# Kernel tuning notes

Hardware: AMD Instinct MI355X
Metric: run time of the kernel (lower is better)

## Reference

```python
import jax, jax.numpy as jnp
import numpy as np

# Config matching init_kwargs: lat_size=512, fin=64, fout=64, fhidden=128,
# dim=2, kernel_size=1, stride=1, padding=0, groups=1, lat_factor=1.
B, FIN, FOUT, FHID, H, W = 16, 64, 64, 128, 128, 128
LAT = 512
LS = 512            # self.lat_size (lat_size > 3 so unchanged) * lat_factor
HID1 = 1024         # LinearResidualBlock default hidden = fin + fout
HID2 = 1024         # second LRB hidden = self.lat_size * lat_factor * 2
SIZES = [FHID*FIN, FHID*FHID, FOUT*FHID, FOUT*FIN, FHID, FHID, FOUT, FOUT]
KTOT = int(np.sum(SIZES))  # 37248
OFFS = np.cumsum([0] + SIZES)


def setup_inputs() -> dict:
    key = jax.random.key(0)
    ks = jax.random.split(key, 10)
    def w(k, shape):
        return (jax.random.normal(k, shape, jnp.float32) / np.sqrt(shape[0])).astype(jnp.float32)
    return {
        "x": jax.random.normal(ks[0], (B, FIN, H, W), jnp.float32),
        "lat": jax.random.normal(ks[1], (B, LAT), jnpp := jnp.float32) if False else jax.random.normal(ks[1], (B, LAT), jnp.float32),
        # dyna_k = Linear(LAT, LS) -> LRB(LS, LS) -> LRB(LS, KTOT, hidden=HID2)
        "dk_w": w(ks[2], (LAT, LS)), "dk_b": jnp.zeros((LS,), jnp.float32),
        "l1_w1": w(ks[3], (LS, HID1)), "l1_b1": jnp.zeros((HID1,), jnp.float32),
        "l1_w2": w(ks[4], (HID1, LS)), "l1_b2": jnp.zeros((LS,), jnp.float32),
        "l2_w1": w(ks[5], (LS, HID2)), "l2_b1": jnp.zeros((HID2,), jnp.float32),
        "l2_w2": w(ks[6], (HID2, KTOT)), "l2_b2": jnp.zeros((KTOT,), jnp.float32),
        "l2_ws": w(ks[7], (LS, KTOT)),  # shortcut linear (fin != fout)
    }


def _lrb(h, w1, b1, w2, b2, ws=None):
    # LinearResidualBlock: shortcut(h) + Linear(ReLU(Linear(h)))
    sc = h if ws is None else h @ ws
    return sc + jax.nn.relu(h @ w1 + b1) @ w2 + b2


def _hyper(lat, dk_w, dk_b, l1_w1, l1_b1, l1_w2, l1_b2, l2_w1, l2_b1, l2_w2, l2_b2, l2_ws):
    h = lat @ dk_w + dk_b
    h = _lrb(h, l1_w1, l1_b1, l1_w2, l1_b2)          # fin == fout -> identity shortcut
    return _lrb(h, l2_w1, l2_b1, l2_w2, l2_b2, l2_ws)


def _dyna_block(x, ksv):
    # Split hypernet output into per-sample 1x1 conv kernels and biases.
    k_in = ksv[:, OFFS[0]:OFFS[1]].reshape(B, FHID, FIN)
    k_mid = ksv[:, OFFS[1]:OFFS[2]].reshape(B, FHID, FHID)
    k_out = ksv[:, OFFS[2]:OFFS[3]].reshape(B, FOUT, FHID)
    k_sh = ksv[:, OFFS[3]:OFFS[4]].reshape(B, FOUT, FIN)
    b_in = ksv[:, OFFS[4]:OFFS[5]][:, :, None, None]
    b_mid = ksv[:, OFFS[5]:OFFS[6]][:, :, None, None]
    b_out = ksv[:, OFFS[6]:OFFS[7]][:, :, None, None]
    b_sh = ksv[:, OFFS[7]:OFFS[8]][:, :, None, None]
    # groups = batch trick == per-sample 1x1 conv == batched channel GEMM
    xs = jnp.einsum('boi,bihw->bohw', k_sh, x) + b_sh
    hh = jax.nn.relu(jnp.einsum('boi,bihw->bohw', k_in, x) + b_in)
    hh = jax.nn.relu(jnp.einsum('boi,bihw->bohw', k_mid, hh) + b_mid)
    return jnp.einsum('boi,bihw->bohw', k_out, hh) + b_out + xs


def reference(x, lat, dk_w, dk_b, l1_w1, l1_b1, l1_w2, l1_b2, l2_w1, l2_b1, l2_w2, l2_b2, l2_ws):
    ksv = _hyper(lat, dk_w, dk_b, l1_w1, l1_b1, l1_w2, l1_b2, l2_w1, l2_b1, l2_w2, l2_b2, l2_ws)
    return _dyna_block(x, ksv)  # [B, FOUT, H, W]
```

## Files before the change

kernel.cpp:

```cpp
#include <hip/hip_runtime.h>

#define N_KSV 37248
#define N_KW  36864

typedef float f32x4 __attribute__((ext_vector_type(4)));
typedef short short8 __attribute__((ext_vector_type(8)));
typedef short short4v __attribute__((ext_vector_type(4)));
typedef __bf16 bf16x8 __attribute__((ext_vector_type(8)));

__device__ inline short f2bs(float f) {
  unsigned u = __builtin_bit_cast(unsigned, f);
  u += 0x7fffu + ((u >> 16) & 1u);
  return (short)(u >> 16);
}

__device__ inline f32x4 ntl4(const float* p) {
  return __builtin_nontemporal_load(reinterpret_cast<const f32x4*>(p));
}

__device__ inline f32x4 mfma16(short8 a, short8 b, f32x4 c) {
  return __builtin_amdgcn_mfma_f32_16x16x32_bf16(
      __builtin_bit_cast(bf16x8, a), __builtin_bit_cast(bf16x8, b), c, 0, 0, 0);
}

__global__ void k_h0(const float* __restrict__ lat, const float* __restrict__ w,
                     const float* __restrict__ bias, float* __restrict__ h0) {
  int j = blockIdx.x * 256 + threadIdx.x;
  int b = blockIdx.y;
  const float* lp = lat + b * 512;
  float acc = bias[j];
#pragma unroll 16
  for (int k = 0; k < 512; ++k) acc = fmaf(lp[k], w[k * 512 + j], acc);
  h0[b * 512 + j] = acc;
}

__global__ void k_t1(const float* __restrict__ h0, const float* __restrict__ w,
                     const float* __restrict__ bias, float* __restrict__ t1) {
  int j = blockIdx.x * 256 + threadIdx.x;
  int b = blockIdx.y;
  const float* hp = h0 + b * 512;
  float acc = bias[j];
#pragma unroll 16
  for (int k = 0; k < 512; ++k) acc = fmaf(hp[k], w[k * 1024 + j], acc);
  t1[b * 1024 + j] = fmaxf(acc, 0.f);
}

__global__ void k_h(const float* __restrict__ h0, const float* __restrict__ t1,
                    const float* __restrict__ w, const float* __restrict__ bias,
                    float* __restrict__ h, short* __restrict__ hxT) {
  int j = blockIdx.x * 256 + threadIdx.x;
  int b = blockIdx.y;
  const float* tp = t1 + b * 1024;
  float acc = bias[j];
#pragma unroll 16
  for (int k = 0; k < 1024; ++k) acc = fmaf(tp[k], w[k * 512 + j], acc);
  float v = acc + h0[b * 512 + j];
  h[b * 512 + j] = v;
  hxT[b * 1536 + j] = f2bs(v);
}

__global__ void k_t2(const float* __restrict__ h, const float* __restrict__ w,
                     const float* __restrict__ bias, short* __restrict__ hxT) {
  int j = blockIdx.x * 256 + threadIdx.x;
  int b = blockIdx.y;
  const float* hp = h + b * 512;
  float acc = bias[j];
#pragma unroll 16
  for (int k = 0; k < 512; ++k) acc = fmaf(hp[k], w[k * 1024 + j], acc);
  hxT[b * 1536 + 512 + j] = f2bs(fmaxf(acc, 0.f));
}

#define LOADB(dst, ktv) { \
    const float* bp_ = ((ktv) < 16) ? (wsp + (size_t)((ktv) * 32) * N_KSV) \
                                    : (w2p + (size_t)((ktv) * 32 - 512) * N_KSV); \
    dst[0] = *reinterpret_cast<const f32x4*>(bp_); \
    dst[1] = *reinterpret_cast<const f32x4*>(bp_ + (size_t)1 * N_KSV); \
    dst[2] = *reinterpret_cast<const f32x4*>(bp_ + (size_t)2 * N_KSV); \
    dst[3] = *reinterpret_cast<const f32x4*>(bp_ + (size_t)3 * N_KSV); \
    dst[4] = *reinterpret_cast<const f32x4*>(bp_ + (size_t)4 * N_KSV); \
    dst[5] = *reinterpret_cast<const f32x4*>(bp_ + (size_t)5 * N_KSV); \
    dst[6] = *reinterpret_cast<const f32x4*>(bp_ + (size_t)6 * N_KSV); \
    dst[7] = *reinterpret_cast<const f32x4*>(bp_ + (size_t)7 * N_KSV); }

#define LOADA(dst, ktv) \
    dst = *reinterpret_cast<const short8*>(apb + (ktv) * 32);

#define COMPUTE(bsrc, asrc) { \
    _Pragma("unroll") \
    for (int t = 0; t < 4; ++t) { \
      short8 bf_; \
      bf_[0] = f2bs(bsrc[0][t]); bf_[1] = f2bs(bsrc[1][t]); \
      bf_[2] = f2bs(bsrc[2][t]); bf_[3] = f2bs(bsrc[3][t]); \
      bf_[4] = f2bs(bsrc[4][t]); bf_[5] = f2bs(bsrc[5][t]); \
      bf_[6] = f2bs(bsrc[6][t]); bf_[7] = f2bs(bsrc[7][t]); \
      acc[t] = mfma16(asrc, bf_, acc[t]); \
    } }

__global__ __launch_bounds__(256, 4) void k5_mfma(
    const float* __restrict__ wsm, const float* __restrict__ w2,
    const short* __restrict__ hxT, const float* __restrict__ b2,
    float* __restrict__ ksv, short* __restrict__ kwb) {
  __shared__ f32x4 red[3][64][4];
  const int tid = threadIdx.x;
  const int wv = tid >> 6;
  const int lane = tid & 63;
  const int col0 = blockIdx.x * 64;
  const int l15 = lane & 15;
  const int lg = lane >> 4;

  const float* wsp = wsm + (size_t)(lg * 8) * N_KSV + col0 + l15 * 4;
  const float* w2p = w2 + (size_t)(lg * 8) * N_KSV + col0 + l15 * 4;
  const short* apb = hxT + l15 * 1536 + lg * 8;

  f32x4 acc[4];
#pragma unroll
  for (int t = 0; t < 4; ++t) acc[t] = (f32x4){0.f, 0.f, 0.f, 0.f};

  const int kt0 = wv * 12;
  f32x4 bA[8], bB[8];
  short8 aA, aB;
  LOADB(bA, kt0);
  LOADA(aA, kt0);

#pragma unroll
  for (int s = 0; s < 12; ++s) {
    if (s + 1 < 12) {
      if ((s & 1) == 0) {
        LOADB(bB, kt0 + s + 1);
        LOADA(aB, kt0 + s + 1);
      } else {
        LOADB(bA, kt0 + s + 1);
        LOADA(aA, kt0 + s + 1);
      }
    }
    if ((s & 1) == 0) COMPUTE(bA, aA) else COMPUTE(bB, aB)
  }

  if (wv > 0) {
#pragma unroll
    for (int t = 0; t < 4; ++t) red[wv - 1][lane][t] = acc[t];
  }
  __syncthreads();
  if (wv != 0) return;

#pragma unroll
  for (int t = 0; t < 4; ++t) {
    acc[t] += red[0][lane][t];
    acc[t] += red[1][lane][t];
    acc[t] += red[2][lane][t];
  }

  const int m0 = lg * 4;
#pragma unroll
  for (int t = 0; t < 4; ++t) {
    const int col = col0 + l15 * 4 + t;
    const float bias = b2[col];
#pragma unroll
    for (int r = 0; r < 4; ++r) {
      float s = acc[t][r] + bias;
      ksv[(size_t)(m0 + r) * N_KSV + col] = s;
      if (col < N_KW)
        kwb[(size_t)(m0 + r) * N_KW + col] = f2bs(s);
    }
  }
}

__device__ inline int xT_idx(int p, int c) {
  return p * 64 + ((((c >> 3) ^ (p & 7)) << 3) | (c & 7));
}
__device__ inline int h_idx(int p, int c) {
  return p * 128 + ((((c >> 3) ^ (p & 7)) << 3) | (c & 7));
}

__device__ __forceinline__ void dyna_L1(const short* xT, short* h1s,
    const short* kw, const float* bias, int w, int l15, int lg) {
  short8 a1[2][2];
#pragma unroll
  for (int mt = 0; mt < 2; ++mt)
#pragma unroll
    for (int kf = 0; kf < 2; ++kf)
      a1[mt][kf] = *reinterpret_cast<const short8*>(
          kw + (w * 32 + mt * 16 + l15) * 64 + kf * 32 + lg * 8);

  f32x4 acc1[2][4];
#pragma unroll
  for (int mt = 0; mt < 2; ++mt)
#pragma unroll
    for (int nt = 0; nt < 4; ++nt) acc1[mt][nt] = (f32x4){0.f, 0.f, 0.f, 0.f};

#pragma unroll
  for (int nt = 0; nt < 4; ++nt) {
    int p = nt * 16 + l15;
    short8 b0 = *reinterpret_cast<const short8*>(&xT[xT_idx(p, lg * 8)]);
    short8 b1 = *reinterpret_cast<const short8*>(&xT[xT_idx(p, 32 + lg * 8)]);
#pragma unroll
    for (int mt = 0; mt < 2; ++mt) {
      acc1[mt][nt] = mfma16(a1[mt][0], b0, acc1[mt][nt]);
      acc1[mt][nt] = mfma16(a1[mt][1], b1, acc1[mt][nt]);
    }
  }
#pragma unroll
  for (int mt = 0; mt < 2; ++mt) {
    int ch0 = w * 32 + mt * 16 + lg * 4;
    f32x4 bv = *reinterpret_cast<const f32x4*>(bias + ch0);
#pragma unroll
    for (int nt = 0; nt < 4; ++nt) {
      int p = nt * 16 + l15;
      short4v hv;
#pragma unroll
      for (int jj = 0; jj < 4; ++jj)
        hv[jj] = f2bs(fmaxf(acc1[mt][nt][jj] + bv[jj], 0.f));
      *reinterpret_cast<short4v*>(&h1s[h_idx(p, ch0)]) = hv;
    }
  }
}

__device__ __forceinline__ void dyna_L2(const short* h1s, short* h2s,
    const short* kw, const float* bias, int w, int l15, int lg) {
  short8 a2[2][4];
#pragma unroll
  for (int mt = 0; mt < 2; ++mt)
#pragma unroll
    for (int kf = 0; kf < 4; ++kf)
      a2[mt][kf] = *reinterpret_cast<const short8*>(
          kw + 8192 + (w * 32 + mt * 16 + l15) * 128 + kf * 32 + lg * 8);

  f32x4 acc2[2][4];
#pragma unroll
  for (int mt = 0; mt < 2; ++mt)
#pragma unroll
    for (int nt = 0; nt < 4; ++nt) acc2[mt][nt] = (f32x4){0.f, 0.f, 0.f, 0.f};

#pragma unroll
  for (int nt = 0; nt < 4; ++nt) {
    int p = nt * 16 + l15;
    short8 bb[4];
#pragma unroll
    for (int kf = 0; kf < 4; ++kf)
      bb[kf] = *reinterpret_cast<const short8*>(&h1s[h_idx(p, kf * 32 + lg * 8)]);
#pragma unroll
    for (int mt = 0; mt < 2; ++mt)
#pragma unroll
      for (int kf = 0; kf < 4; ++kf)
        acc2[mt][nt] = mfma16(a2[mt][kf], bb[kf], acc2[mt][nt]);
  }
#pragma unroll
  for (int mt = 0; mt < 2; ++mt) {
    int ch0 = w * 32 + mt * 16 + lg * 4;
    f32x4 bv = *reinterpret_cast<const f32x4*>(bias + 128 + ch0);
#pragma unroll
    for (int nt = 0; nt < 4; ++nt) {
      int p = nt * 16 + l15;
      short4v hv;
#pragma unroll
      for (int jj = 0; jj < 4; ++jj)
        hv[jj] = f2bs(fmaxf(acc2[mt][nt][jj] + bv[jj], 0.f));
      *reinterpret_cast<short4v*>(&h2s[h_idx(p, ch0)]) = hv;
    }
  }
}

__device__ __forceinline__ void dyna_L3(const short* h2s, const short* xT,
    const short* kw, const float* bias, float* outb, int pos0,
    int w, int l15, int lg) {
  short8 a3[4], ash[2];
#pragma unroll
  for (int kf = 0; kf < 4; ++kf)
    a3[kf] = *reinterpret_cast<const short8*>(
        kw + 24576 + (w * 16 + l15) * 128 + kf * 32 + lg * 8);
#pragma unroll
  for (int kf = 0; kf < 2; ++kf)
    ash[kf] = *reinterpret_cast<const short8*>(
        kw + 32768 + (w * 16 + l15) * 64 + kf * 32 + lg * 8);

  int ch0 = w * 16 + lg * 4;
  f32x4 bo = *reinterpret_cast<const f32x4*>(bias + 256 + ch0);
  f32x4 bs = *reinterpret_cast<const f32x4*>(bias + 320 + ch0);

#pragma unroll
  for (int nt = 0; nt < 4; ++nt) {
    int p = nt * 16 + l15;
    f32x4 acc = {0.f, 0.f, 0.f, 0.f};
#pragma unroll
    for (int kf = 0; kf < 4; ++kf) {
      short8 bb = *reinterpret_cast<const short8*>(&h2s[h_idx(p, kf * 32 + lg * 8)]);
      acc = mfma16(a3[kf], bb, acc);
    }
#pragma unroll
    for (int kf = 0; kf < 2; ++kf) {
      short8 bb = *reinterpret_cast<const short8*>(&xT[xT_idx(p, kf * 32 + lg * 8)]);
      acc = mfma16(ash[kf], bb, acc);
    }
#pragma unroll
    for (int jj = 0; jj < 4; ++jj)
      __builtin_nontemporal_store(acc[jj] + bo[jj] + bs[jj],
          outb + (((size_t)(ch0 + jj)) << 14) + pos0 + p);
  }
}

__global__ __launch_bounds__(256) void k_dyna(const float* __restrict__ x,
                                              const short* __restrict__ kwb,
                                              const float* __restrict__ ksv,
                                              float* __restrict__ out) {
  __shared__ __align__(16) short lds[24576];
  short* xTA = lds;
  short* xTB = lds + 4096;
  short* h1s = lds + 8192;
  short* h2s = lds + 16384;

  const int tid = threadIdx.x;
  const int lane = tid & 63;
  const int w = tid >> 6;
  const int l15 = lane & 15;
  const int lg = lane >> 4;

  const int b = blockIdx.x >> 7;
  const int pos0A = (blockIdx.x & 127) << 7;
  const int pos0B = pos0A + 64;

  const float* xb = x + ((size_t)b << 20);
  const short* kw = kwb + b * N_KW;
  const float* bias = ksv + (size_t)b * N_KSV + N_KW;
  float* outb = out + ((size_t)b << 20);

  const int cc = (tid >> 3) * 2;
  const int p0 = (tid & 7) * 8;
  const float* xrow = xb + (size_t)cc * 16384 + p0;

  f32x4 a0 = ntl4(xrow + pos0A),        a1v = ntl4(xrow + pos0A + 4);
  f32x4 a2v = ntl4(xrow + 16384 + pos0A), a3v = ntl4(xrow + 16384 + pos0A + 4);
  f32x4 b0 = ntl4(xrow + pos0B),        b1v = ntl4(xrow + pos0B + 4);
  f32x4 b2v = ntl4(xrow + 16384 + pos0B), b3v = ntl4(xrow + 16384 + pos0B + 4);

#define WRITEX(xT, r0, r1, r2, r3) { \
    _Pragma("unroll") \
    for (int i = 0; i < 8; ++i) { \
      float va = (i < 4) ? r0[i] : r1[i - 4]; \
      float vb = (i < 4) ? r2[i] : r3[i - 4]; \
      int pk = (int)(unsigned short)f2bs(va) | ((int)f2bs(vb) << 16); \
      *reinterpret_cast<int*>(&(xT)[xT_idx(p0 + i, cc)]) = pk; \
    } }

  WRITEX(xTA, a0, a1v, a2v, a3v);
  __syncthreads();

  dyna_L1(xTA, h1s, kw, bias, w, l15, lg);
  __syncthreads();
  dyna_L2(h1s, h2s, kw, bias, w, l15, lg);
  WRITEX(xTB, b0, b1v, b2v, b3v);
  __syncthreads();
  dyna_L3(h2s, xTA, kw, bias, outb, pos0A, w, l15, lg);
  dyna_L1(xTB, h1s, kw, bias, w, l15, lg);
  __syncthreads();
  dyna_L2(h1s, h2s, kw, bias, w, l15, lg);
  __syncthreads();
  dyna_L3(h2s, xTB, kw, bias, outb, pos0B, w, l15, lg);
#undef WRITEX
}

extern "C" void kernel_launch(void* const* d_in, const int* in_sizes, int n_in,
                              void* d_out, int out_size, void* d_ws, size_t ws_size,
                              hipStream_t stream) {
  const float* x    = (const float*)d_in[0];
  const float* lat  = (const float*)d_in[1];
  const float* dk_w = (const float*)d_in[2];
  const float* dk_b = (const float*)d_in[3];
  const float* l1w1 = (const float*)d_in[4];
  const float* l1b1 = (const float*)d_in[5];
  const float* l1w2 = (const float*)d_in[6];
  const float* l1b2 = (const float*)d_in[7];
  const float* l2w1 = (const float*)d_in[8];
  const float* l2b1 = (const float*)d_in[9];
  const float* l2w2 = (const float*)d_in[10];
  const float* l2b2 = (const float*)d_in[11];
  const float* l2ws = (const float*)d_in[12];
  float* out = (float*)d_out;
  float* wsf = (float*)d_ws;

  float* h0  = wsf;
  float* t1  = wsf + 8192;
  float* h   = wsf + 24576;
  float* ksv = wsf + 32768;
  short* hxT = (short*)(wsf + 628736);
  short* kwb = hxT + 24576;

  k_h0<<<dim3(2, 16), 256, 0, stream>>>(lat, dk_w, dk_b, h0);
  k_t1<<<dim3(4, 16), 256, 0, stream>>>(h0, l1w1, l1b1, t1);
  k_h <<<dim3(2, 16), 256, 0, stream>>>(h0, t1, l1w2, l1b2, h, hxT);
  k_t2<<<dim3(4, 16), 256, 0, stream>>>(h, l2w1, l2b1, hxT);
  k5_mfma<<<dim3(N_KSV / 64), 256, 0, stream>>>(l2ws, l2w2, hxT, l2b2, ksv, kwb);
  k_dyna<<<dim3(2048), 256, 0, stream>>>(x, kwb, ksv, out);
}
```

Measured before the change: 191.7 us.

## Process four 64-position tiles per block in the dynamic conv kernel

Each k_dyna block now handles 256 spatial positions (four 64-wide tiles) instead of 128, and the grid is halved. All x data for the block is loaded and converted to bf16 up front into a larger shared staging buffer, then the three per-sample GEMM layers are run once per tile in a loop. The aim is to spread the per-block setup cost over more work and to issue all global loads together. In exchange, shared memory per block grows from 48KB to 64KB, which can lower blocks per CU. Each thread also holds 64 floats in registers, and the earlier overlap of loading the second tile while computing the first is lost.

```diff
diff --git a/kernel.cpp b/kernel.cpp
--- a/kernel.cpp
+++ b/kernel.cpp
@@ -302,11 +302,10 @@
                                               const short* __restrict__ kwb,
                                               const float* __restrict__ ksv,
                                               float* __restrict__ out) {
-  __shared__ __align__(16) short lds[24576];
-  short* xTA = lds;
-  short* xTB = lds + 4096;
-  short* h1s = lds + 8192;
-  short* h2s = lds + 16384;
+  __shared__ __align__(16) short lds[32768];
+  short* xT4 = lds;
+  short* h1s = lds + 16384;
+  short* h2s = lds + 24576;
 
   const int tid = threadIdx.x;
   const int lane = tid & 63;
@@ -314,48 +313,44 @@
   const int l15 = lane & 15;
   const int lg = lane >> 4;
 
-  const int b = blockIdx.x >> 7;
-  const int pos0A = (blockIdx.x & 127) << 7;
-  const int pos0B = pos0A + 64;
+  const int b = blockIdx.x >> 6;
+  const int pos0 = (blockIdx.x & 63) << 8;
 
   const float* xb = x + ((size_t)b << 20);
   const short* kw = kwb + b * N_KW;
   const float* bias = ksv + (size_t)b * N_KSV + N_KW;
   float* outb = out + ((size_t)b << 20);
 
-  const int cc = (tid >> 3) * 2;
-  const int p0 = (tid & 7) * 8;
-  const float* xrow = xb + (size_t)cc * 16384 + p0;
-
-  f32x4 a0 = ntl4(xrow + pos0A),        a1v = ntl4(xrow + pos0A + 4);
-  f32x4 a2v = ntl4(xrow + 16384 + pos0A), a3v = ntl4(xrow + 16384 + pos0A + 4);
-  f32x4 b0 = ntl4(xrow + pos0B),        b1v = ntl4(xrow + pos0B + 4);
-  f32x4 b2v = ntl4(xrow + 16384 + pos0B), b3v = ntl4(xrow + 16384 + pos0B + 4);
-
-#define WRITEX(xT, r0, r1, r2, r3) { \
-    _Pragma("unroll") \
-    for (int i = 0; i < 8; ++i) { \
-      float va = (i < 4) ? r0[i] : r1[i - 4]; \
-      float vb = (i < 4) ? r2[i] : r3[i - 4]; \
-      int pk = (int)(unsigned short)f2bs(va) | ((int)f2bs(vb) << 16); \
-      *reinterpret_cast<int*>(&(xT)[xT_idx(p0 + i, cc)]) = pk; \
-    } }
-
-  WRITEX(xTA, a0, a1v, a2v, a3v);
+  {
+    const int cc = (tid >> 3) * 2;
+    const int pc = (tid & 7) * 32;
+    const float* r0 = xb + (size_t)cc * 16384 + pos0 + pc;
+    const float* r1 = r0 + 16384;
+    f32x4 v0[8], v1[8];
+#pragma unroll
+    for (int i = 0; i < 8; ++i) v0[i] = ntl4(r0 + i * 4);
+#pragma unroll
+    for (int i = 0; i < 8; ++i) v1[i] = ntl4(r1 + i * 4);
+#pragma unroll
+    for (int p = 0; p < 32; ++p) {
+      int gp = pc + p;
+      int tile = gp >> 6, pp = gp & 63;
+      int pk = (int)(unsigned short)f2bs(v0[p >> 2][p & 3]) |
+               ((int)f2bs(v1[p >> 2][p & 3]) << 16);
+      *reinterpret_cast<int*>(&xT4[tile * 4096 + xT_idx(pp, cc)]) = pk;
+    }
+  }
   __syncthreads();
 
-  dyna_L1(xTA, h1s, kw, bias, w, l15, lg);
-  __syncthreads();
-  dyna_L2(h1s, h2s, kw, bias, w, l15, lg);
-  WRITEX(xTB, b0, b1v, b2v, b3v);
-  __syncthreads();
-  dyna_L3(h2s, xTA, kw, bias, outb, pos0A, w, l15, lg);
-  dyna_L1(xTB, h1s, kw, bias, w, l15, lg);
-  __syncthreads();
-  dyna_L2(h1s, h2s, kw, bias, w, l15, lg);
-  __syncthreads();
-  dyna_L3(h2s, xTB, kw, bias, outb, pos0B, w, l15, lg);
-#undef WRITEX
+#pragma unroll
+  for (int t = 0; t < 4; ++t) {
+    const short* xT = xT4 + t * 4096;
+    dyna_L1(xT, h1s, kw, bias, w, l15, lg);
+    __syncthreads();
+    dyna_L2(h1s, h2s, kw, bias, w, l15, lg);
+    __syncthreads();
+    dyna_L3(h2s, xT, kw, bias, outb, pos0 + t * 64, w, l15, lg);
+  }
 }
 
 extern "C" void kernel_launch(void* const* d_in, const int* in_sizes, int n_in,
@@ -389,5 +384,5 @@
   k_h <<<dim3(2, 16), 256, 0, stream>>>(h0, t1, l1w2, l1b2, h, hxT);
   k_t2<<<dim3(4, 16), 256, 0, stream>>>(h, l2w1, l2b1, hxT);
   k5_mfma<<<dim3(N_KSV / 64), 256, 0, stream>>>(l2ws, l2w2, hxT, l2b2, ksv, kwb);
-  k_dyna<<<dim3(2048), 256, 0, stream>>>(x, kwb, ksv, out);
-}
+  k_dyna<<<dim3(1024), 256, 0, stream>>>(x, kwb, ksv, out);
+}
```

Result: slower. 217.5 us (+13.4%).
